# Optimization experiments

Hardware: AMD Instinct MI355X
Metric: run time of the kernel (lower is better)

## Reference

```python
import jax, jax.numpy as jnp
import numpy as np

B, T, D, H = 2, 2048, 1024, 16
HD = D // H  # 64


def setup_inputs() -> dict:
    key = jax.random.key(0)
    ks = jax.random.split(key, 9)
    w = lambda k, shp: (jax.random.normal(k, shp, jnp.float32) * 0.02)
    return {
        "x": jax.random.normal(ks[0], (B, T, D), jnp.float32),
        "Wq": w(ks[1], (D, D)), "bq": jnp.zeros((D,), jnp.float32),
        "Wk": w(ks[2], (D, D)), "bk": jnp.zeros((D,), jnp.float32),
        "Wv": w(ks[3], (D, D)), "bv": jnp.zeros((D,), jnp.float32),
        "Wo": w(ks[4], (D, D)), "bo": jnp.zeros((D,), jnp.float32),
        "Wqs": w(ks[5], (3, HD)), "bqs": jnp.zeros((3,), jnp.float32),
        "Wks": w(ks[6], (3, HD)), "bks": jnp.zeros((3,), jnp.float32),
        "Wvs": w(ks[7], (3, HD)), "bvs": jnp.zeros((3,), jnp.float32),
        "temp": jnp.float32(1.0),
    }


def reference(x, Wq, bq, Wk, bk, Wv, bv, Wo, bo, Wqs, bqs, Wks, bks, Wvs, bvs, temp):
    Bx, Tx, Dx = x.shape
    # project and split heads: [B,H,T,HD]
    split = lambda y: y.reshape(Bx, Tx, H, HD).transpose(0, 2, 1, 3)
    q = split(x @ Wq.T + bq)
    k = split(x @ Wk.T + bk)
    v = split(x @ Wv.T + bv)
    # STP projections to 3-d: [B,H,T,3]
    q_stp = q @ Wqs.T + bqs
    k3 = k @ Wks.T + bks
    v3 = v @ Wvs.T + bvs
    # cross-product term (note: original's layernormed k_sub/v_sub are dead code)
    cross_kv = jnp.cross(k3, v3, axis=-1)  # [B,H,T,3]
    scores = (jnp.einsum('bhqd,bhkd->bhqk', q, k)
              + jnp.einsum('bhqc,bhkc->bhqk', q_stp, cross_kv)) * temp
    attn = jax.nn.softmax(scores, axis=-1)
    out = jnp.einsum('bhqk,bhkd->bhqd', attn, v)  # [B,H,T,HD]
    out = out.transpose(0, 2, 1, 3).reshape(Bx, Tx, Dx)
    return out @ Wo.T + bo
```

## Files before the change

kernel.cpp:

```cpp
#include <hip/hip_runtime.h>
#include <stdint.h>

typedef unsigned short u16;
typedef unsigned int u32;
typedef __attribute__((ext_vector_type(8))) short bf16x8;
typedef __attribute__((ext_vector_type(4))) float f32x4;
typedef __attribute__((ext_vector_type(4))) unsigned int u32x4;

__device__ __forceinline__ u16 f2b(float f) {
    union { float f; u32 u; } t; t.f = f;
    return (u16)((t.u + 0x7FFFu + ((t.u >> 16) & 1u)) >> 16);
}
__device__ __forceinline__ u32 pack2(float a, float b) {
    return (u32)f2b(a) | ((u32)f2b(b) << 16);
}
__device__ __forceinline__ u32 cvtpk2(float lo, float hi) {
    u32 r;
    asm("v_cvt_pk_bf16_f32 %0, %1, %2" : "=v"(r) : "v"(lo), "v"(hi));
    return r;
}
__device__ __forceinline__ void permlane32_swap(u32& a, u32& b) {
    asm("v_permlane32_swap_b32 %0, %1" : "+v"(a), "+v"(b));
}
__device__ __forceinline__ void permlane16_swap(u32& a, u32& b) {
    asm("v_permlane16_swap_b32 %0, %1" : "+v"(a), "+v"(b));
}

__device__ __forceinline__ void async_cp16(const u16* g, const u16* lds_base) {
    __builtin_amdgcn_global_load_lds(
        (const __attribute__((address_space(1))) void*)(uintptr_t)g,
        (__attribute__((address_space(3))) void*)(u32)(uintptr_t)lds_base,
        16, 0, 0);
}

__global__ void cast_all_kernel(const float* __restrict__ x,
                                const float* __restrict__ Wq, const float* __restrict__ Wk,
                                const float* __restrict__ Wv, const float* __restrict__ Wo,
                                u16* __restrict__ xb, u16* __restrict__ Wqb, u16* __restrict__ Wkb,
                                u16* __restrict__ Wvb, u16* __restrict__ Wob) {
    int i = blockIdx.x * blockDim.x + threadIdx.x;
    const float* s; u16* d; int off;
    if (i < 1048576) { s = x; d = xb; off = i; }
    else {
        int j = i - 1048576;
        int w = j >> 18; off = j & 262143;
        if (w == 0) { s = Wq; d = Wqb; }
        else if (w == 1) { s = Wk; d = Wkb; }
        else if (w == 2) { s = Wv; d = Wvb; }
        else { s = Wo; d = Wob; }
    }
    float4 f = ((const float4*)s)[off];
    ((uint2*)d)[off] = make_uint2(pack2(f.x, f.y), pack2(f.z, f.w));
}

__global__ __launch_bounds__(256) void gemm_qkv_kernel(
    const u16* __restrict__ xb,
    const u16* __restrict__ Wq, const u16* __restrict__ Wk, const u16* __restrict__ Wv,
    const float* __restrict__ bq, const float* __restrict__ bk, const float* __restrict__ bv,
    const float* __restrict__ Wqs, const float* __restrict__ bqs,
    const float* __restrict__ Wks, const float* __restrict__ bks,
    const float* __restrict__ Wvs, const float* __restrict__ bvs,
    const float* __restrict__ temp_p,
    u16* __restrict__ qe, u16* __restrict__ ke, u16* __restrict__ vT,
    float4* __restrict__ k3b, float4* __restrict__ v3b)
{
    __shared__ __align__(16) u16 As[2 * 128 * 32];
    __shared__ __align__(16) u16 Bs[2 * 128 * 32];
    const int tid = threadIdx.x;
    const int lane = tid & 63, w = tid >> 6;
    const int wm = w >> 1, wn = w & 1;
    const int l15 = lane & 15, quad = lane >> 4;
    const int lin = blockIdx.x;
    const int M0 = (lin & 31) * 128;
    const int N0 = ((lin >> 5) & 7) * 128;
    const int bz = lin >> 8;

    const u16* W = (bz == 0) ? Wq : (bz == 1) ? Wk : Wv;
    const float* bias = (bz == 0) ? bq : (bz == 1) ? bk : bv;
    const float* Wst = (bz == 0) ? Wqs : (bz == 1) ? Wks : Wvs;
    const float* bst = (bz == 0) ? bqs : (bz == 1) ? bks : bvs;

    f32x4 acc[4][4];
#pragma unroll
    for (int i = 0; i < 4; i++)
#pragma unroll
        for (int j = 0; j < 4; j++) acc[i][j] = (f32x4){0.f, 0.f, 0.f, 0.f};

    const int ca2 = ((lane & 3) ^ ((lane >> 2) & 3)) * 8;
    const u16* Ag = xb + (size_t)(M0 + w * 32 + (lane >> 2)) * 1024 + ca2;
    const u16* Bg = W + (size_t)(N0 + w * 32 + (lane >> 2)) * 1024 + ca2;
    const int dst0 = w * 1024;
    const int dst1 = w * 1024 + 512;

    async_cp16(Ag, As + dst0);
    async_cp16(Ag + 16 * 1024, As + dst1);
    async_cp16(Bg, Bs + dst0);
    async_cp16(Bg + 16 * 1024, Bs + dst1);
    __syncthreads();

    for (int k0 = 0; k0 < 1024; k0 += 32) {
        const int buf = (k0 >> 5) & 1;
        const u16* Asr = As + buf * 4096;
        const u16* Bsr = Bs + buf * 4096;
        if (k0 + 32 < 1024) {
            const int nb_ = (buf ^ 1) * 4096;
            async_cp16(Ag + k0 + 32, As + nb_ + dst0);
            async_cp16(Ag + 16 * 1024 + k0 + 32, As + nb_ + dst1);
            async_cp16(Bg + k0 + 32, Bs + nb_ + dst0);
            async_cp16(Bg + 16 * 1024 + k0 + 32, Bs + nb_ + dst1);
        }

        bf16x8 af[4], bf[4];
#pragma unroll
        for (int mi = 0; mi < 4; mi++)
            af[mi] = *(const bf16x8*)(Asr + (wm * 64 + mi * 16 + l15) * 32 + ((quad ^ (l15 & 3)) * 8));
#pragma unroll
        for (int ni = 0; ni < 4; ni++)
            bf[ni] = *(const bf16x8*)(Bsr + (wn * 64 + ni * 16 + l15) * 32 + ((quad ^ (l15 & 3)) * 8));
#pragma unroll
        for (int mi = 0; mi < 4; mi++)
#pragma unroll
            for (int ni = 0; ni < 4; ni++)
                acc[mi][ni] = __builtin_amdgcn_mfma_f32_16x16x32_bf16(af[mi], bf[ni], acc[mi][ni], 0, 0, 0);

        __syncthreads();
    }

    const float tau = temp_p[0] * 1.44269504088896f;
    const int nb = N0 + wn * 64;
    const int h = nb >> 6;
    float bias_v[4], wst_v[3][4];
#pragma unroll
    for (int ni = 0; ni < 4; ni++) {
        bias_v[ni] = bias[nb + ni * 16 + l15];
#pragma unroll
        for (int c = 0; c < 3; c++) wst_v[c][ni] = Wst[c * 64 + ni * 16 + l15];
    }
    const float bst0 = bst[0], bst1 = bst[1], bst2 = bst[2];

#pragma unroll
    for (int mi = 0; mi < 4; mi++) {
        int m0 = M0 + wm * 64 + mi * 16 + quad * 4;
        int b = m0 >> 11, t0 = m0 & 2047;
        float p0[4], p1[4], p2[4];
#pragma unroll
        for (int r = 0; r < 4; r++) {
            float a0 = 0.f, a1 = 0.f, a2 = 0.f;
#pragma unroll
            for (int ni = 0; ni < 4; ni++) {
                float v = acc[mi][ni][r] + bias_v[ni];
                a0 += v * wst_v[0][ni];
                a1 += v * wst_v[1][ni];
                a2 += v * wst_v[2][ni];
            }
#pragma unroll
            for (int off = 1; off < 16; off <<= 1) {
                a0 += __shfl_xor(a0, off);
                a1 += __shfl_xor(a1, off);
                a2 += __shfl_xor(a2, off);
            }
            p0[r] = a0 + bst0; p1[r] = a1 + bst1; p2[r] = a2 + bst2;
        }

        if (bz == 0) {
#pragma unroll
            for (int r = 0; r < 4; r++) {
                size_t row = (size_t)((b * 16 + h) * 2048 + (t0 + r));
                u16* qer = qe + row * 96;
#pragma unroll
                for (int ni = 0; ni < 4; ni++)
                    qer[ni * 16 + l15] = f2b((acc[mi][ni][r] + bias_v[ni]) * tau);
                if (l15 == 0) {
                    *(u32*)(qer + 64) = pack2(p0[r] * tau, p1[r] * tau);
                    *(u32*)(qer + 66) = (u32)f2b(p2[r] * tau);
                    uint2 z = make_uint2(0u, 0u);
#pragma unroll
                    for (int j = 68; j < 96; j += 4) *(uint2*)(qer + j) = z;
                }
            }
        } else if (bz == 1) {
#pragma unroll
            for (int r = 0; r < 4; r++) {
                size_t row = (size_t)((b * 16 + h) * 2048 + (t0 + r));
                u16* ker = ke + row * 96;
#pragma unroll
                for (int ni = 0; ni < 4; ni++)
                    ker[ni * 16 + l15] = f2b(acc[mi][ni][r] + bias_v[ni]);
                if (l15 == 0)
                    k3b[row] = make_float4(p0[r], p1[r], p2[r], 0.f);
            }
        } else {
#pragma unroll
            for (int ni = 0; ni < 4; ni++) {
                int hd = ni * 16 + l15;
                float v0 = acc[mi][ni][0] + bias_v[ni];
                float v1 = acc[mi][ni][1] + bias_v[ni];
                float v2 = acc[mi][ni][2] + bias_v[ni];
                float v3 = acc[mi][ni][3] + bias_v[ni];
                *(uint2*)(vT + ((size_t)((b * 16 + h) * 64 + hd)) * 2048 + t0) =
                    make_uint2(pack2(v0, v1), pack2(v2, v3));
            }
            if (l15 == 0) {
#pragma unroll
                for (int r = 0; r < 4; r++) {
                    size_t row = (size_t)((b * 16 + h) * 2048 + (t0 + r));
                    v3b[row] = make_float4(p0[r], p1[r], p2[r], 0.f);
                }
            }
        }
    }
}

__global__ void finish_ext_kernel(const float4* __restrict__ k3b, const float4* __restrict__ v3b,
                                  u16* __restrict__ ke)
{
    int row = blockIdx.x * blockDim.x + threadIdx.x;
    if (row >= 2 * 16 * 2048) return;
    float4 k3 = k3b[row];
    float4 v3 = v3b[row];
    float c0 = k3.y * v3.z - k3.z * v3.y;
    float c1 = k3.z * v3.x - k3.x * v3.z;
    float c2 = k3.x * v3.y - k3.y * v3.x;
    u16* ker = ke + (size_t)row * 96;
    *(u32*)(ker + 64) = pack2(c0, c1);
    *(u32*)(ker + 66) = (u32)f2b(c2);
    uint2 z = make_uint2(0u, 0u);
#pragma unroll
    for (int j = 68; j < 96; j += 4) *(uint2*)(ker + j) = z;
}

__global__ __launch_bounds__(256) void gemm_out_kernel(
    const u16* __restrict__ ao, const u16* __restrict__ Wo, const float* __restrict__ bo,
    float* __restrict__ out)
{
    __shared__ __align__(16) u16 As[2 * 64 * 32];
    __shared__ __align__(16) u16 Bs[2 * 128 * 32];
    const int tid = threadIdx.x;
    const int lane = tid & 63, w = tid >> 6;
    const int wm = w >> 1, wn = w & 1;
    const int l15 = lane & 15, quad = lane >> 4;
    const int lin = blockIdx.x;
    const int M0 = (lin & 63) * 64;
    const int N0 = (lin >> 6) * 128;

    f32x4 acc[2][4];
#pragma unroll
    for (int i = 0; i < 2; i++)
#pragma unroll
        for (int j = 0; j < 4; j++) acc[i][j] = (f32x4){0.f, 0.f, 0.f, 0.f};

    int ra = tid >> 2, ca = ((tid & 3) ^ (ra & 3)) * 8;
    const u16* Aga = ao + (size_t)(M0 + ra) * 1024 + ca;
    const u16* Bg0 = Wo + (size_t)(N0 + ra) * 1024 + ca;
    const u16* Bg1 = Wo + (size_t)(N0 + ra + 64) * 1024 + ca;
    const int aoff = (w * 64) * 8;
    const int boff0 = (w * 64) * 8;
    const int boff1 = (256 + w * 64) * 8;

    async_cp16(Aga, As + aoff);
    async_cp16(Bg0, Bs + boff0);
    async_cp16(Bg1, Bs + boff1);
    __syncthreads();

    for (int k0 = 0; k0 < 1024; k0 += 32) {
        const int buf = (k0 >> 5) & 1;
        const u16* Asr = As + buf * 2048;
        const u16* Bsr = Bs + buf * 4096;
        if (k0 + 32 < 1024) {
            const int nb_ = buf ^ 1;
            async_cp16(Aga + k0 + 32, As + nb_ * 2048 + aoff);
            async_cp16(Bg0 + k0 + 32, Bs + nb_ * 4096 + boff0);
            async_cp16(Bg1 + k0 + 32, Bs + nb_ * 4096 + boff1);
        }

        bf16x8 af[2], bf[4];
#pragma unroll
        for (int mi = 0; mi < 2; mi++)
            af[mi] = *(const bf16x8*)(Asr + (wm * 32 + mi * 16 + l15) * 32 + ((quad ^ (l15 & 3)) * 8));
#pragma unroll
        for (int ni = 0; ni < 4; ni++)
            bf[ni] = *(const bf16x8*)(Bsr + (wn * 64 + ni * 16 + l15) * 32 + ((quad ^ (l15 & 3)) * 8));
#pragma unroll
        for (int mi = 0; mi < 2; mi++)
#pragma unroll
            for (int ni = 0; ni < 4; ni++)
                acc[mi][ni] = __builtin_amdgcn_mfma_f32_16x16x32_bf16(af[mi], bf[ni], acc[mi][ni], 0, 0, 0);

        __syncthreads();
    }

#pragma unroll
    for (int mi = 0; mi < 2; mi++)
#pragma unroll
        for (int ni = 0; ni < 4; ni++) {
            int n = N0 + wn * 64 + ni * 16 + l15;
            float bias_n = bo[n];
            int m0 = M0 + wm * 32 + mi * 16 + quad * 4;
#pragma unroll
            for (int r = 0; r < 4; r++)
                out[(size_t)(m0 + r) * 1024 + n] = acc[mi][ni][r] + bias_n;
        }
}

__global__ __launch_bounds__(512, 2) void attn_kernel(
    const u16* __restrict__ qe, const u16* __restrict__ ke, const u16* __restrict__ vT,
    u16* __restrict__ out)
{
    __shared__ __align__(16) u16 smem[24576];
    u16* const KsA = smem;
    u16* const VtA = smem + 16384;

    const int tid = threadIdx.x;
    const int lane = tid & 63, w = tid >> 6;
    const int kw = w & 1, qw = w >> 1;
    const int l15 = lane & 15, quad = lane >> 4;
    const int lsw = l15 & 7;
    const int lin = blockIdx.x;
    const int bh = (lin & 7) + ((lin >> 3) & 3) * 8;
    const int q0 = (lin >> 5) * 128;

    const u16* qeb = qe + (size_t)bh * 2048 * 96;
    const u16* keb = ke + (size_t)bh * 2048 * 96;
    const u16* vTb = vT + (size_t)bh * 64 * 2048;

    u32 koff[2];
#pragma unroll
    for (int j = 0; j < 2; j++) {
        int r = w * 8 + j * 4 + (lane >> 4);
        int c = (lane & 15) ^ (r & 7);
        if (c >= 12) c -= 8;
        koff[j] = (u32)(r * 96 + c * 8);
    }
    u32 voff;
    {
        int r = w * 8 + (lane >> 3);
        voff = (u32)(r * 2048 + (((lane & 7) ^ (r & 7)) * 8));
    }

#pragma unroll
    for (int j = 0; j < 2; j++) async_cp16(keb + koff[j], KsA + w * 1024 + j * 512);
    async_cp16(vTb + voff, VtA + w * 512);

    bf16x8 bq[2][3];
#pragma unroll
    for (int s = 0; s < 2; s++) {
        const u16* qrow = qeb + (size_t)(q0 + qw * 32 + s * 16 + l15) * 96;
#pragma unroll
        for (int ks = 0; ks < 3; ks++) bq[s][ks] = *(const bf16x8*)(qrow + ks * 32 + quad * 8);
    }

    f32x4 O[2][4];
    float l_part[2];
#pragma unroll
    for (int s = 0; s < 2; s++) {
        l_part[s] = 0.f;
#pragma unroll
        for (int dt = 0; dt < 4; dt++) O[s][dt] = (f32x4){0.f, 0.f, 0.f, 0.f};
    }

    __syncthreads();

    for (int kb = 0; kb < 2048; kb += 64) {
        const int buf = (kb >> 6) & 1;
        const u16* Ks = KsA + buf * 8192;
        const u16* Vt = VtA + buf * 4096;

        if (kb + 64 < 2048) {
            u16* Ksn = KsA + (buf ^ 1) * 8192;
            u16* Vtn = VtA + (buf ^ 1) * 4096;
            const size_t kb96 = (size_t)(kb + 64) * 96;
#pragma unroll
            for (int j = 0; j < 2; j++) async_cp16(keb + kb96 + koff[j], Ksn + w * 1024 + j * 512);
            async_cp16(vTb + (size_t)(kb + 64) + voff, Vtn + w * 512);
        }

        f32x4 S[2][2];
#pragma unroll
        for (int s = 0; s < 2; s++)
#pragma unroll
            for (int nt = 0; nt < 2; nt++) S[s][nt] = (f32x4){0.f, 0.f, 0.f, 0.f};

        __builtin_amdgcn_s_setprio(1);
#pragma unroll
        for (int ks = 0; ks < 3; ks++) {
            bf16x8 ak[2];
#pragma unroll
            for (int nt = 0; nt < 2; nt++)
                ak[nt] = *(const bf16x8*)(Ks + (kw * 32 + nt * 16 + l15) * 128 + (((ks * 4 + quad) ^ lsw) & 15) * 8);
#pragma unroll
            for (int s = 0; s < 2; s++)
#pragma unroll
                for (int nt = 0; nt < 2; nt++)
                    S[s][nt] = __builtin_amdgcn_mfma_f32_16x16x32_bf16(ak[nt], bq[s][ks], S[s][nt], 0, 0, 0);
        }
        __builtin_amdgcn_s_setprio(0);

        bf16x8 av[4];
#pragma unroll
        for (int dt = 0; dt < 4; dt++)
            av[dt] = *(const bf16x8*)(Vt + (dt * 16 + l15) * 64 + (((kw * 4 + quad) ^ lsw) & 7) * 8);

#pragma unroll
        for (int s = 0; s < 2; s++) {
            float sum = 0.f;
#pragma unroll
            for (int nt = 0; nt < 2; nt++)
#pragma unroll
                for (int r = 0; r < 4; r++) {
                    float p = __builtin_amdgcn_exp2f(S[s][nt][r]);
                    S[s][nt][r] = p;
                    sum += p;
                }
            l_part[s] += sum;
            u32 a0 = cvtpk2(S[s][0][0], S[s][0][1]);
            u32 b0 = cvtpk2(S[s][1][0], S[s][1][1]);
            u32 a1 = cvtpk2(S[s][0][2], S[s][0][3]);
            u32 b1 = cvtpk2(S[s][1][2], S[s][1][3]);
            permlane32_swap(a0, b0);
            permlane32_swap(a1, b1);
            permlane16_swap(a0, b0);
            permlane16_swap(a1, b1);
            bf16x8 pv = __builtin_bit_cast(bf16x8, (u32x4){a0, a1, b0, b1});
            __builtin_amdgcn_s_setprio(1);
#pragma unroll
            for (int dt = 0; dt < 4; dt++)
                O[s][dt] = __builtin_amdgcn_mfma_f32_16x16x32_bf16(av[dt], pv, O[s][dt], 0, 0, 0);
            __builtin_amdgcn_s_setprio(0);
        }

        __syncthreads();
    }

    float* const Ored = (float*)smem;
    float* const Lr = (float*)(smem + 17664);
    if (kw == 1) {
#pragma unroll
        for (int s = 0; s < 2; s++) {
            float l = l_part[s];
            l += __shfl_xor(l, 16);
            l += __shfl_xor(l, 32);
            int qrow = qw * 32 + s * 16 + l15;
            if (lane < 16) Lr[qrow] = l;
#pragma unroll
            for (int dt = 0; dt < 4; dt++) {
                int dc = dt ^ (l15 & 3);
                *(float4*)(Ored + qrow * 68 + dc * 16 + quad * 4) =
                    make_float4(O[s][dt][0], O[s][dt][1], O[s][dt][2], O[s][dt][3]);
            }
        }
    }
    __syncthreads();
    if (kw == 0) {
        const int b = bh >> 4, h = bh & 15;
#pragma unroll
        for (int s = 0; s < 2; s++) {
            float l = l_part[s];
            l += __shfl_xor(l, 16);
            l += __shfl_xor(l, 32);
            int qrow = qw * 32 + s * 16 + l15;
            l += Lr[qrow];
            float linv = 1.0f / l;
            int tq = q0 + qrow;
#pragma unroll
            for (int dt = 0; dt < 4; dt++) {
                int dc = dt ^ (l15 & 3);
                float4 o2 = *(const float4*)(Ored + qrow * 68 + dc * 16 + quad * 4);
                int d = h * 64 + dt * 16 + quad * 4;
                *(uint2*)(out + (size_t)(b * 2048 + tq) * 1024 + d) =
                    make_uint2(cvtpk2((O[s][dt][0] + o2.x) * linv, (O[s][dt][1] + o2.y) * linv),
                               cvtpk2((O[s][dt][2] + o2.z) * linv, (O[s][dt][3] + o2.w) * linv));
            }
        }
    }
}

extern "C" void kernel_launch(void* const* d_in, const int* in_sizes, int n_in,
                              void* d_out, int out_size, void* d_ws, size_t ws_size,
                              hipStream_t stream)
{
    (void)in_sizes; (void)n_in; (void)out_size; (void)ws_size;
    const float* x   = (const float*)d_in[0];
    const float* Wq  = (const float*)d_in[1];
    const float* bq  = (const float*)d_in[2];
    const float* Wk  = (const float*)d_in[3];
    const float* bk  = (const float*)d_in[4];
    const float* Wv  = (const float*)d_in[5];
    const float* bv  = (const float*)d_in[6];
    const float* Wo  = (const float*)d_in[7];
    const float* bo  = (const float*)d_in[8];
    const float* Wqs = (const float*)d_in[9];
    const float* bqs = (const float*)d_in[10];
    const float* Wks = (const float*)d_in[11];
    const float* bks = (const float*)d_in[12];
    const float* Wvs = (const float*)d_in[13];
    const float* bvs = (const float*)d_in[14];
    const float* temp = (const float*)d_in[15];

    char* ws = (char*)d_ws;
    u16* xb  = (u16*)(ws);
    u16* Wqb = (u16*)(ws + 8388608);
    u16* Wkb = (u16*)(ws + 10485760);
    u16* Wvb = (u16*)(ws + 12582912);
    u16* Wob = (u16*)(ws + 14680064);
    u16* qeb = (u16*)(ws + 16777216);
    u16* keb = (u16*)(ws + 29360128);
    u16* vTb = (u16*)(ws + 41943040);
    float4* k3b = (float4*)(ws + 50331648);
    float4* v3b = (float4*)(ws + 51380224);
    u16* aob = (u16*)(ws + 52428800);

    cast_all_kernel<<<8192, 256, 0, stream>>>(x, Wq, Wk, Wv, Wo, xb, Wqb, Wkb, Wvb, Wob);
    gemm_qkv_kernel<<<768, 256, 0, stream>>>(
        xb, Wqb, Wkb, Wvb, bq, bk, bv, Wqs, bqs, Wks, bks, Wvs, bvs, temp,
        qeb, keb, vTb, k3b, v3b);
    finish_ext_kernel<<<256, 256, 0, stream>>>(k3b, v3b, keb);
    attn_kernel<<<512, 512, 0, stream>>>(qeb, keb, vTb, aob);
    gemm_out_kernel<<<512, 256, 0, stream>>>(aob, Wob, bo, (float*)d_out);
}
```

Baseline: 208.6 us.

## Use 64-wide K tiles in both GEMMs and shrink QKV M-tile to 64

Both projection GEMMs now stage 64-element K slices per iteration instead of 32, with a new 8-way XOR swizzle, halving the number of barrier-separated iterations. The QKV GEMM tile shrinks from 128x128 to 64x128, doubling the grid to 1536 blocks for better CU occupancy and load balance. The cost is more LDS per block, and the smaller QKV tile gives less operand reuse and more global traffic.

```diff
diff --git a/kernel.cpp b/kernel.cpp
--- a/kernel.cpp
+++ b/kernel.cpp
@@ -64,64 +64,81 @@
     u16* __restrict__ qe, u16* __restrict__ ke, u16* __restrict__ vT,
     float4* __restrict__ k3b, float4* __restrict__ v3b)
 {
-    __shared__ __align__(16) u16 As[2 * 128 * 32];
-    __shared__ __align__(16) u16 Bs[2 * 128 * 32];
+    __shared__ __align__(16) u16 As[2 * 64 * 64];
+    __shared__ __align__(16) u16 Bs[2 * 128 * 64];
     const int tid = threadIdx.x;
     const int lane = tid & 63, w = tid >> 6;
     const int wm = w >> 1, wn = w & 1;
     const int l15 = lane & 15, quad = lane >> 4;
     const int lin = blockIdx.x;
-    const int M0 = (lin & 31) * 128;
-    const int N0 = ((lin >> 5) & 7) * 128;
-    const int bz = lin >> 8;
+    const int M0 = (lin & 63) * 64;
+    const int N0 = ((lin >> 6) & 7) * 128;
+    const int bz = lin >> 9;
 
     const u16* W = (bz == 0) ? Wq : (bz == 1) ? Wk : Wv;
     const float* bias = (bz == 0) ? bq : (bz == 1) ? bk : bv;
     const float* Wst = (bz == 0) ? Wqs : (bz == 1) ? Wks : Wvs;
     const float* bst = (bz == 0) ? bqs : (bz == 1) ? bks : bvs;
 
-    f32x4 acc[4][4];
-#pragma unroll
-    for (int i = 0; i < 4; i++)
+    f32x4 acc[2][4];
+#pragma unroll
+    for (int i = 0; i < 2; i++)
 #pragma unroll
         for (int j = 0; j < 4; j++) acc[i][j] = (f32x4){0.f, 0.f, 0.f, 0.f};
 
-    const int ca2 = ((lane & 3) ^ ((lane >> 2) & 3)) * 8;
-    const u16* Ag = xb + (size_t)(M0 + w * 32 + (lane >> 2)) * 1024 + ca2;
-    const u16* Bg = W + (size_t)(N0 + w * 32 + (lane >> 2)) * 1024 + ca2;
-    const int dst0 = w * 1024;
-    const int dst1 = w * 1024 + 512;
-
-    async_cp16(Ag, As + dst0);
-    async_cp16(Ag + 16 * 1024, As + dst1);
-    async_cp16(Bg, Bs + dst0);
-    async_cp16(Bg + 16 * 1024, Bs + dst1);
+    const int lr3 = lane >> 3, lp = lane & 7;
+    u32 aoff[2];
+#pragma unroll
+    for (int j = 0; j < 2; j++) {
+        int r = w * 16 + j * 8 + lr3;
+        aoff[j] = (u32)(r * 1024 + ((lp ^ (r & 7)) * 8));
+    }
+    u32 boff[4];
+#pragma unroll
+    for (int j = 0; j < 4; j++) {
+        int r = w * 32 + j * 8 + lr3;
+        boff[j] = (u32)(r * 1024 + ((lp ^ (r & 7)) * 8));
+    }
+    const u16* Ag = xb + (size_t)M0 * 1024;
+    const u16* Bg = W + (size_t)N0 * 1024;
+
+#pragma unroll
+    for (int j = 0; j < 2; j++) async_cp16(Ag + aoff[j], As + w * 1024 + j * 512);
+#pragma unroll
+    for (int j = 0; j < 4; j++) async_cp16(Bg + boff[j], Bs + w * 2048 + j * 512);
     __syncthreads();
 
-    for (int k0 = 0; k0 < 1024; k0 += 32) {
-        const int buf = (k0 >> 5) & 1;
+    for (int k0 = 0; k0 < 1024; k0 += 64) {
+        const int buf = (k0 >> 6) & 1;
         const u16* Asr = As + buf * 4096;
-        const u16* Bsr = Bs + buf * 4096;
-        if (k0 + 32 < 1024) {
-            const int nb_ = (buf ^ 1) * 4096;
-            async_cp16(Ag + k0 + 32, As + nb_ + dst0);
-            async_cp16(Ag + 16 * 1024 + k0 + 32, As + nb_ + dst1);
-            async_cp16(Bg + k0 + 32, Bs + nb_ + dst0);
-            async_cp16(Bg + 16 * 1024 + k0 + 32, Bs + nb_ + dst1);
-        }
-
-        bf16x8 af[4], bf[4];
-#pragma unroll
-        for (int mi = 0; mi < 4; mi++)
-            af[mi] = *(const bf16x8*)(Asr + (wm * 64 + mi * 16 + l15) * 32 + ((quad ^ (l15 & 3)) * 8));
-#pragma unroll
-        for (int ni = 0; ni < 4; ni++)
-            bf[ni] = *(const bf16x8*)(Bsr + (wn * 64 + ni * 16 + l15) * 32 + ((quad ^ (l15 & 3)) * 8));
-#pragma unroll
-        for (int mi = 0; mi < 4; mi++)
-#pragma unroll
-            for (int ni = 0; ni < 4; ni++)
-                acc[mi][ni] = __builtin_amdgcn_mfma_f32_16x16x32_bf16(af[mi], bf[ni], acc[mi][ni], 0, 0, 0);
+        const u16* Bsr = Bs + buf * 8192;
+        if (k0 + 64 < 1024) {
+            const int nb_ = buf ^ 1;
+#pragma unroll
+            for (int j = 0; j < 2; j++) async_cp16(Ag + (k0 + 64) + aoff[j], As + nb_ * 4096 + w * 1024 + j * 512);
+#pragma unroll
+            for (int j = 0; j < 4; j++) async_cp16(Bg + (k0 + 64) + boff[j], Bs + nb_ * 8192 + w * 2048 + j * 512);
+        }
+
+#pragma unroll
+        for (int kk = 0; kk < 2; kk++) {
+            bf16x8 af[2], bf[4];
+#pragma unroll
+            for (int mi = 0; mi < 2; mi++) {
+                int ra = wm * 32 + mi * 16 + l15;
+                af[mi] = *(const bf16x8*)(Asr + ra * 64 + (((kk * 4 + quad) ^ (ra & 7)) * 8));
+            }
+#pragma unroll
+            for (int ni = 0; ni < 4; ni++) {
+                int rb = wn * 64 + ni * 16 + l15;
+                bf[ni] = *(const bf16x8*)(Bsr + rb * 64 + (((kk * 4 + quad) ^ (rb & 7)) * 8));
+            }
+#pragma unroll
+            for (int mi = 0; mi < 2; mi++)
+#pragma unroll
+                for (int ni = 0; ni < 4; ni++)
+                    acc[mi][ni] = __builtin_amdgcn_mfma_f32_16x16x32_bf16(af[mi], bf[ni], acc[mi][ni], 0, 0, 0);
+        }
 
         __syncthreads();
     }
@@ -139,8 +156,8 @@
     const float bst0 = bst[0], bst1 = bst[1], bst2 = bst[2];
 
 #pragma unroll
-    for (int mi = 0; mi < 4; mi++) {
-        int m0 = M0 + wm * 64 + mi * 16 + quad * 4;
+    for (int mi = 0; mi < 2; mi++) {
+        int m0 = M0 + wm * 32 + mi * 16 + quad * 4;
         int b = m0 >> 11, t0 = m0 & 2047;
         float p0[4], p1[4], p2[4];
 #pragma unroll
@@ -233,8 +250,8 @@
     const u16* __restrict__ ao, const u16* __restrict__ Wo, const float* __restrict__ bo,
     float* __restrict__ out)
 {
-    __shared__ __align__(16) u16 As[2 * 64 * 32];
-    __shared__ __align__(16) u16 Bs[2 * 128 * 32];
+    __shared__ __align__(16) u16 As[2 * 64 * 64];
+    __shared__ __align__(16) u16 Bs[2 * 128 * 64];
     const int tid = threadIdx.x;
     const int lane = tid & 63, w = tid >> 6;
     const int wm = w >> 1, wn = w & 1;
@@ -249,42 +266,59 @@
 #pragma unroll
         for (int j = 0; j < 4; j++) acc[i][j] = (f32x4){0.f, 0.f, 0.f, 0.f};
 
-    int ra = tid >> 2, ca = ((tid & 3) ^ (ra & 3)) * 8;
-    const u16* Aga = ao + (size_t)(M0 + ra) * 1024 + ca;
-    const u16* Bg0 = Wo + (size_t)(N0 + ra) * 1024 + ca;
-    const u16* Bg1 = Wo + (size_t)(N0 + ra + 64) * 1024 + ca;
-    const int aoff = (w * 64) * 8;
-    const int boff0 = (w * 64) * 8;
-    const int boff1 = (256 + w * 64) * 8;
-
-    async_cp16(Aga, As + aoff);
-    async_cp16(Bg0, Bs + boff0);
-    async_cp16(Bg1, Bs + boff1);
+    const int lr3 = lane >> 3, lp = lane & 7;
+    u32 aoff[2];
+#pragma unroll
+    for (int j = 0; j < 2; j++) {
+        int r = w * 16 + j * 8 + lr3;
+        aoff[j] = (u32)(r * 1024 + ((lp ^ (r & 7)) * 8));
+    }
+    u32 boff[4];
+#pragma unroll
+    for (int j = 0; j < 4; j++) {
+        int r = w * 32 + j * 8 + lr3;
+        boff[j] = (u32)(r * 1024 + ((lp ^ (r & 7)) * 8));
+    }
+    const u16* Ag = ao + (size_t)M0 * 1024;
+    const u16* Bg = Wo + (size_t)N0 * 1024;
+
+#pragma unroll
+    for (int j = 0; j < 2; j++) async_cp16(Ag + aoff[j], As + w * 1024 + j * 512);
+#pragma unroll
+    for (int j = 0; j < 4; j++) async_cp16(Bg + boff[j], Bs + w * 2048 + j * 512);
     __syncthreads();
 
-    for (int k0 = 0; k0 < 1024; k0 += 32) {
-        const int buf = (k0 >> 5) & 1;
-        const u16* Asr = As + buf * 2048;
-        const u16* Bsr = Bs + buf * 4096;
-        if (k0 + 32 < 1024) {
+    for (int k0 = 0; k0 < 1024; k0 += 64) {
+        const int buf = (k0 >> 6) & 1;
+        const u16* Asr = As + buf * 4096;
+        const u16* Bsr = Bs + buf * 8192;
+        if (k0 + 64 < 1024) {
             const int nb_ = buf ^ 1;
-            async_cp16(Aga + k0 + 32, As + nb_ * 2048 + aoff);
-            async_cp16(Bg0 + k0 + 32, Bs + nb_ * 4096 + boff0);
-            async_cp16(Bg1 + k0 + 32, Bs + nb_ * 4096 + boff1);
-        }
-
-        bf16x8 af[2], bf[4];
-#pragma unroll
-        for (int mi = 0; mi < 2; mi++)
-            af[mi] = *(const bf16x8*)(Asr + (wm * 32 + mi * 16 + l15) * 32 + ((quad ^ (l15 & 3)) * 8));
-#pragma unroll
-        for (int ni = 0; ni < 4; ni++)
-            bf[ni] = *(const bf16x8*)(Bsr + (wn * 64 + ni * 16 + l15) * 32 + ((quad ^ (l15 & 3)) * 8));
-#pragma unroll
-        for (int mi = 0; mi < 2; mi++)
-#pragma unroll
-            for (int ni = 0; ni < 4; ni++)
-                acc[mi][ni] = __builtin_amdgcn_mfma_f32_16x16x32_bf16(af[mi], bf[ni], acc[mi][ni], 0, 0, 0);
+#pragma unroll
+            for (int j = 0; j < 2; j++) async_cp16(Ag + (k0 + 64) + aoff[j], As + nb_ * 4096 + w * 1024 + j * 512);
+#pragma unroll
+            for (int j = 0; j < 4; j++) async_cp16(Bg + (k0 + 64) + boff[j], Bs + nb_ * 8192 + w * 2048 + j * 512);
+        }
+
+#pragma unroll
+        for (int kk = 0; kk < 2; kk++) {
+            bf16x8 af[2], bf[4];
+#pragma unroll
+            for (int mi = 0; mi < 2; mi++) {
+                int ra = wm * 32 + mi * 16 + l15;
+                af[mi] = *(const bf16x8*)(Asr + ra * 64 + (((kk * 4 + quad) ^ (ra & 7)) * 8));
+            }
+#pragma unroll
+            for (int ni = 0; ni < 4; ni++) {
+                int rb = wn * 64 + ni * 16 + l15;
+                bf[ni] = *(const bf16x8*)(Bsr + rb * 64 + (((kk * 4 + quad) ^ (rb & 7)) * 8));
+            }
+#pragma unroll
+            for (int mi = 0; mi < 2; mi++)
+#pragma unroll
+                for (int ni = 0; ni < 4; ni++)
+                    acc[mi][ni] = __builtin_amdgcn_mfma_f32_16x16x32_bf16(af[mi], bf[ni], acc[mi][ni], 0, 0, 0);
+        }
 
         __syncthreads();
     }
@@ -510,7 +544,7 @@
     u16* aob = (u16*)(ws + 52428800);
 
     cast_all_kernel<<<8192, 256, 0, stream>>>(x, Wq, Wk, Wv, Wo, xb, Wqb, Wkb, Wvb, Wob);
-    gemm_qkv_kernel<<<768, 256, 0, stream>>>(
+    gemm_qkv_kernel<<<1536, 256, 0, stream>>>(
         xb, Wqb, Wkb, Wvb, bq, bk, bv, Wqs, bqs, Wks, bks, Wvs, bvs, temp,
         qeb, keb, vTb, k3b, v3b);
     finish_ext_kernel<<<256, 256, 0, stream>>>(k3b, v3b, keb);
```

After: 205.8 us. About the same (-1.4%).
